# Performance work log

Hardware: AMD Instinct MI355X
Metric: run time of the kernel (lower is better)

The kernel has to match this reference:

```python
import jax, jax.numpy as jnp
import numpy as np

RADIUS = 0.1
NSAMPLE = 64


def ball_query(xyz, new_xyz, pointsnum, radius, nsample):
    """xyz (B,N,2), new_xyz (B,S,2), pointsnum (B,) -> idx (B,S,nsample) int32.
    Mirrors CUDA ball_query: for each query take the first `nsample` point
    indices (in index order) whose squared distance < radius^2 and index <
    pointsnum[b]; slots beyond the number found are padded with the first
    found index (0 if none found)."""
    N = xyz.shape[1]
    # (B,S,N) squared distances
    d2 = jnp.sum((new_xyz[:, :, None, :] - xyz[:, None, :, :]) ** 2, axis=-1)
    valid = jnp.arange(N, dtype=jnp.int32)[None, None, :] < pointsnum[:, None, None]
    mask = (d2 < radius * radius) & valid
    # key = point index if in ball else N (sentinel); smallest `nsample` keys
    key = jnp.where(mask, jnp.arange(N, dtype=jnp.int32), N)
    neg_small, _ = jax.lax.top_k(-key, nsample)          # largest of -key == smallest keys
    sorted_keys = -neg_small                              # ascending in-ball indices, N-padded
    first = sorted_keys[..., :1]
    pad = jnp.where(first < N, first, 0)
    idx = jnp.where(sorted_keys < N, sorted_keys, pad)
    return idx.astype(jnp.int32)


def group(features, idx):
    """features (B,C,N), idx (B,S,K) -> (B,C,S,K)."""
    return jax.vmap(lambda f, i: f[:, i])(features, idx)


def setup_inputs() -> dict:
    key = jax.random.key(0)
    k1, k2, k3 = jax.random.split(key, 3)
    B, N, S, C = 4, 16384, 2048, 64
    xyz = jax.random.uniform(k1, (B, N, 2), dtype=jnp.float32)
    new_xyz = jax.random.uniform(k2, (B, S, 2), dtype=jnp.float32)
    features = jax.random.normal(k3, (B, C, N), dtype=jnp.float32)
    pointsnum = jnp.full((B,), N, dtype=jnp.int32)
    return {"xyz": xyz, "new_xyz": new_xyz, "features": features, "pointsnum": pointsnum}


def reference(xyz, new_xyz, features, pointsnum):
    # QueryAndGroup(radius=RADIUS, nsample=NSAMPLE, use_xyz=True)
    idx = ball_query(xyz, new_xyz, pointsnum, RADIUS, NSAMPLE)  # (B,S,K) int32
    xyz_t = jnp.transpose(xyz, (0, 2, 1))                        # (B,2,N)
    grouped_xyz = group(xyz_t, idx)                              # (B,2,S,K)
    grouped_xyz = grouped_xyz - jnp.transpose(new_xyz, (0, 2, 1))[..., None]
    grouped_features = group(features, idx)                      # (B,C,S,K)
    new_features = jnp.concatenate([grouped_xyz, grouped_features], axis=1)  # (B,2+C,S,K)
    return new_features
```

## Files before the change

### kernel.cpp

```cpp
#include <hip/hip_runtime.h>
#include <stdint.h>

#define B 4
#define N 16384
#define S 2048
#define C 64
#define K 64
#define OC 66
#define R2 0.01f
#define NXCD 8

typedef float f32x4 __attribute__((ext_vector_type(4)));

__global__ __launch_bounds__(256) void transpose_kernel(const float* __restrict__ f,
                                                        float* __restrict__ ft) {
    __shared__ float tile[64 * 65];
    const int n0 = blockIdx.x * 64;
    const int b  = blockIdx.y;
    const int t  = threadIdx.x;

    const int nl = t & 63, cl = t >> 6;
    #pragma unroll
    for (int cc = cl; cc < 64; cc += 4) {
        tile[cc * 65 + nl] = __builtin_nontemporal_load(&f[((size_t)b * C + cc) * N + n0 + nl]);
    }
    __syncthreads();

    const int cl2 = t & 63, nl2 = t >> 6;
    #pragma unroll
    for (int nn = nl2; nn < 64; nn += 4) {
        ft[((size_t)b * N + n0 + nn) * C + cl2] = tile[cl2 * 65 + nn];
    }
}

template <bool USE_T>
__global__ __launch_bounds__(256) void qag_kernel(const float* __restrict__ xyz,
                                                  const float* __restrict__ new_xyz,
                                                  const float* __restrict__ feat,
                                                  const float* __restrict__ ft,
                                                  const int* __restrict__ pointsnum,
                                                  float* __restrict__ out) {
    __shared__ int   s_idx[4][K];
    __shared__ float tile[4][16][K];

    const int t    = threadIdx.x;
    const int lane = t & 63;
    const int wu   = __builtin_amdgcn_readfirstlane(t >> 6);

    const int nwg = (B * S) / 4;
    const int bid = blockIdx.x;
    const int swz = (bid & (NXCD - 1)) * (nwg / NXCD) + (bid >> 3);

    const int q0   = swz * 4;
    const int b    = q0 >> 11;
    const int s0   = q0 & (S - 1);
    const int q    = q0 + wu;
    const int s    = s0 + wu;

    const float qx = new_xyz[(size_t)q * 2 + 0];
    const float qy = new_xyz[(size_t)q * 2 + 1];
    const float* __restrict__ xb = xyz + (size_t)b * N * 2;

    int pn = pointsnum[b];
    pn = pn < 0 ? 0 : (pn > N ? N : pn);
    int cnt = 0;
    for (int base = 0; base < pn && cnt < K; base += 256) {
        float2 p[4];
        #pragma unroll
        for (int u = 0; u < 4; ++u) {
            int i  = base + u * 64 + lane;
            int ic = i < N ? i : N - 1;
            p[u] = *(const float2*)&xb[(size_t)ic * 2];
        }
        #pragma unroll
        for (int u = 0; u < 4; ++u) {
            const int i = base + u * 64 + lane;
            bool ok = false;
            if (i < pn) {
                const float dx = __fsub_rn(qx, p[u].x);
                const float dy = __fsub_rn(qy, p[u].y);
                const float d2 = __fadd_rn(__fmul_rn(dx, dx), __fmul_rn(dy, dy));
                ok = d2 < R2;
            }
            const unsigned long long m = __ballot(ok);
            if (ok) {
                const int pos = cnt + __popcll(m & ((1ull << lane) - 1ull));
                if (pos < K) s_idx[wu][pos] = i;
            }
            cnt += __popcll(m);
        }
    }
    const int found = cnt < K ? cnt : K;
    const int first = (found > 0) ? s_idx[wu][0] : 0;
    const int id    = (lane < found) ? s_idx[wu][lane] : first;

    const size_t SK = (size_t)S * K;
    const float2 pxy = *(const float2*)&xb[(size_t)id * 2];
    {
        float* ob = out + ((size_t)b * OC) * SK + (size_t)s * K;
        __builtin_nontemporal_store(pxy.x - qx, ob + lane);
        __builtin_nontemporal_store(pxy.y - qy, ob + SK + lane);
    }

    const float* __restrict__ row = USE_T ? (ft + ((size_t)b * N + id) * C) : nullptr;
    const float* __restrict__ fb  = feat + (size_t)b * C * N;
    const int ql = lane >> 4;
    const int kq = (lane & 15) * 4;

    #pragma unroll
    for (int cc = 0; cc < 4; ++cc) {
        float4 g0, g1, g2, g3;
        if (USE_T) {
            const float4* r4 = (const float4*)(row + 16 * cc);
            g0 = r4[0]; g1 = r4[1]; g2 = r4[2]; g3 = r4[3];
        } else {
            const int c0 = 16 * cc;
            g0.x = fb[(size_t)(c0 +  0) * N + id]; g0.y = fb[(size_t)(c0 +  1) * N + id];
            g0.z = fb[(size_t)(c0 +  2) * N + id]; g0.w = fb[(size_t)(c0 +  3) * N + id];
            g1.x = fb[(size_t)(c0 +  4) * N + id]; g1.y = fb[(size_t)(c0 +  5) * N + id];
            g1.z = fb[(size_t)(c0 +  6) * N + id]; g1.w = fb[(size_t)(c0 +  7) * N + id];
            g2.x = fb[(size_t)(c0 +  8) * N + id]; g2.y = fb[(size_t)(c0 +  9) * N + id];
            g2.z = fb[(size_t)(c0 + 10) * N + id]; g2.w = fb[(size_t)(c0 + 11) * N + id];
            g3.x = fb[(size_t)(c0 + 12) * N + id]; g3.y = fb[(size_t)(c0 + 13) * N + id];
            g3.z = fb[(size_t)(c0 + 14) * N + id]; g3.w = fb[(size_t)(c0 + 15) * N + id];
        }

        __syncthreads();
        tile[wu][ 0][lane] = g0.x; tile[wu][ 1][lane] = g0.y;
        tile[wu][ 2][lane] = g0.z; tile[wu][ 3][lane] = g0.w;
        tile[wu][ 4][lane] = g1.x; tile[wu][ 5][lane] = g1.y;
        tile[wu][ 6][lane] = g1.z; tile[wu][ 7][lane] = g1.w;
        tile[wu][ 8][lane] = g2.x; tile[wu][ 9][lane] = g2.y;
        tile[wu][10][lane] = g2.z; tile[wu][11][lane] = g2.w;
        tile[wu][12][lane] = g3.x; tile[wu][13][lane] = g3.y;
        tile[wu][14][lane] = g3.z; tile[wu][15][lane] = g3.w;
        __syncthreads();

        #pragma unroll
        for (int j = 0; j < 4; ++j) {
            const int c16 = 4 * wu + j;
            const int c   = 16 * cc + c16;
            f32x4 vv = *(const f32x4*)&tile[ql][c16][kq];
            float* bp = out + ((size_t)b * OC + 2 + c) * SK + (size_t)s0 * K;
            __builtin_nontemporal_store(vv, ((f32x4*)bp) + lane);
        }
    }
}

extern "C" void kernel_launch(void* const* d_in, const int* in_sizes, int n_in,
                              void* d_out, int out_size, void* d_ws, size_t ws_size,
                              hipStream_t stream) {
    const float* xyz       = (const float*)d_in[0];
    const float* new_xyz   = (const float*)d_in[1];
    const float* feat      = (const float*)d_in[2];
    const int*   pointsnum = (const int*)d_in[3];
    float*       out       = (float*)d_out;

    const size_t need = (size_t)B * N * C * sizeof(float);
    if (ws_size >= need) {
        float* ft = (float*)d_ws;
        transpose_kernel<<<dim3(N / 64, B), 256, 0, stream>>>(feat, ft);
        qag_kernel<true><<<B * S / 4, 256, 0, stream>>>(xyz, new_xyz, feat, ft, pointsnum, out);
    } else {
        qag_kernel<false><<<B * S / 4, 256, 0, stream>>>(xyz, new_xyz, feat, nullptr, pointsnum, out);
    }
}
```

Before: 55.91 us.

## Overlap ball query with feature transpose in one prep kernel, gather separately

Merges the feature transpose and the ball-query search into a single prep launch: blocks below 1024 transpose features, and the remaining blocks run the neighbor search and write relative xyz plus the index list to the workspace. A separate gather kernel then reads the indices and scatters the transposed feature rows into the output. The aim is to run the compute-bound search alongside the bandwidth-bound transpose instead of serialising them. The cost is an extra index round-trip through global memory and one more launch boundary before the gather.

```diff
diff --git a/kernel.cpp b/kernel.cpp
--- a/kernel.cpp
+++ b/kernel.cpp
@@ -12,24 +12,139 @@
 
 typedef float f32x4 __attribute__((ext_vector_type(4)));
 
-__global__ __launch_bounds__(256) void transpose_kernel(const float* __restrict__ f,
-                                                        float* __restrict__ ft) {
+__global__ __launch_bounds__(256) void prep_kernel(const float* __restrict__ f,
+                                                   const float* __restrict__ xyz,
+                                                   const float* __restrict__ new_xyz,
+                                                   const int* __restrict__ pointsnum,
+                                                   float* __restrict__ ft,
+                                                   int* __restrict__ idx,
+                                                   float* __restrict__ out) {
     __shared__ float tile[64 * 65];
-    const int n0 = blockIdx.x * 64;
-    const int b  = blockIdx.y;
-    const int t  = threadIdx.x;
-
-    const int nl = t & 63, cl = t >> 6;
+    __shared__ int   s_idx[4][K];
+
+    const int t = threadIdx.x;
+
+    if (blockIdx.x < 1024) {
+        const int n0 = (blockIdx.x & 255) * 64;
+        const int b  = blockIdx.x >> 8;
+
+        const int nl = t & 63, cl = t >> 6;
+        #pragma unroll
+        for (int cc = cl; cc < 64; cc += 4) {
+            tile[cc * 65 + nl] = __builtin_nontemporal_load(&f[((size_t)b * C + cc) * N + n0 + nl]);
+        }
+        __syncthreads();
+
+        const int cl2 = t & 63, nl2 = t >> 6;
+        #pragma unroll
+        for (int nn = nl2; nn < 64; nn += 4) {
+            ft[((size_t)b * N + n0 + nn) * C + cl2] = tile[cl2 * 65 + nn];
+        }
+        return;
+    }
+
+    const int lane = t & 63;
+    const int wu   = __builtin_amdgcn_readfirstlane(t >> 6);
+    const int q0   = (int)(blockIdx.x - 1024) * 4;
+    const int b    = q0 >> 11;
+    const int q    = q0 + wu;
+    const int s    = (q0 & (S - 1)) + wu;
+
+    const float qx = new_xyz[(size_t)q * 2 + 0];
+    const float qy = new_xyz[(size_t)q * 2 + 1];
+    const float* __restrict__ xb = xyz + (size_t)b * N * 2;
+
+    int pn = pointsnum[b];
+    pn = pn < 0 ? 0 : (pn > N ? N : pn);
+    int cnt = 0;
+    for (int base = 0; base < pn && cnt < K; base += 256) {
+        float2 p[4];
+        #pragma unroll
+        for (int u = 0; u < 4; ++u) {
+            int i  = base + u * 64 + lane;
+            int ic = i < N ? i : N - 1;
+            p[u] = *(const float2*)&xb[(size_t)ic * 2];
+        }
+        #pragma unroll
+        for (int u = 0; u < 4; ++u) {
+            const int i = base + u * 64 + lane;
+            bool ok = false;
+            if (i < pn) {
+                const float dx = __fsub_rn(qx, p[u].x);
+                const float dy = __fsub_rn(qy, p[u].y);
+                const float d2 = __fadd_rn(__fmul_rn(dx, dx), __fmul_rn(dy, dy));
+                ok = d2 < R2;
+            }
+            const unsigned long long m = __ballot(ok);
+            if (ok) {
+                const int pos = cnt + __popcll(m & ((1ull << lane) - 1ull));
+                if (pos < K) s_idx[wu][pos] = i;
+            }
+            cnt += __popcll(m);
+        }
+    }
+    const int found = cnt < K ? cnt : K;
+    const int first = (found > 0) ? s_idx[wu][0] : 0;
+    const int id    = (lane < found) ? s_idx[wu][lane] : first;
+
+    idx[(size_t)q * K + lane] = id;
+
+    const size_t SK = (size_t)S * K;
+    const float2 pxy = *(const float2*)&xb[(size_t)id * 2];
+    float* ob = out + ((size_t)b * OC) * SK + (size_t)s * K;
+    __builtin_nontemporal_store(pxy.x - qx, ob + lane);
+    __builtin_nontemporal_store(pxy.y - qy, ob + SK + lane);
+}
+
+__global__ __launch_bounds__(256) void gather_kernel(const float* __restrict__ ft,
+                                                     const int* __restrict__ idx,
+                                                     float* __restrict__ out) {
+    __shared__ float tile[4][16][K];
+
+    const int t    = threadIdx.x;
+    const int lane = t & 63;
+    const int wu   = __builtin_amdgcn_readfirstlane(t >> 6);
+
+    const int nwg = (B * S) / 4;
+    const int bid = blockIdx.x;
+    const int swz = (bid & (NXCD - 1)) * (nwg / NXCD) + (bid >> 3);
+
+    const int q0 = swz * 4;
+    const int b  = q0 >> 11;
+    const int s0 = q0 & (S - 1);
+    const int q  = q0 + wu;
+
+    const int id = idx[(size_t)q * K + lane];
+    const float* __restrict__ row = ft + ((size_t)b * N + id) * C;
+
+    const size_t SK = (size_t)S * K;
+    const int ql = lane >> 4;
+    const int kq = (lane & 15) * 4;
+
     #pragma unroll
-    for (int cc = cl; cc < 64; cc += 4) {
-        tile[cc * 65 + nl] = __builtin_nontemporal_load(&f[((size_t)b * C + cc) * N + n0 + nl]);
-    }
-    __syncthreads();
-
-    const int cl2 = t & 63, nl2 = t >> 6;
-    #pragma unroll
-    for (int nn = nl2; nn < 64; nn += 4) {
-        ft[((size_t)b * N + n0 + nn) * C + cl2] = tile[cl2 * 65 + nn];
+    for (int cc = 0; cc < 4; ++cc) {
+        const float4* r4 = (const float4*)(row + 16 * cc);
+        const float4 g0 = r4[0], g1 = r4[1], g2 = r4[2], g3 = r4[3];
+
+        __syncthreads();
+        tile[wu][ 0][lane] = g0.x; tile[wu][ 1][lane] = g0.y;
+        tile[wu][ 2][lane] = g0.z; tile[wu][ 3][lane] = g0.w;
+        tile[wu][ 4][lane] = g1.x; tile[wu][ 5][lane] = g1.y;
+        tile[wu][ 6][lane] = g1.z; tile[wu][ 7][lane] = g1.w;
+        tile[wu][ 8][lane] = g2.x; tile[wu][ 9][lane] = g2.y;
+        tile[wu][10][lane] = g2.z; tile[wu][11][lane] = g2.w;
+        tile[wu][12][lane] = g3.x; tile[wu][13][lane] = g3.y;
+        tile[wu][14][lane] = g3.z; tile[wu][15][lane] = g3.w;
+        __syncthreads();
+
+        #pragma unroll
+        for (int j = 0; j < 4; ++j) {
+            const int c16 = 4 * wu + j;
+            const int c   = 16 * cc + c16;
+            f32x4 vv = *(const f32x4*)&tile[ql][c16][kq];
+            float* bp = out + ((size_t)b * OC + 2 + c) * SK + (size_t)s0 * K;
+            __builtin_nontemporal_store(vv, ((f32x4*)bp) + lane);
+        }
     }
 }
 
@@ -156,10 +271,17 @@
     const int*   pointsnum = (const int*)d_in[3];
     float*       out       = (float*)d_out;
 
-    const size_t need = (size_t)B * N * C * sizeof(float);
-    if (ws_size >= need) {
+    const size_t ft_bytes  = (size_t)B * N * C * sizeof(float);
+    const size_t idx_bytes = (size_t)B * S * K * sizeof(int);
+
+    if (ws_size >= ft_bytes + idx_bytes) {
+        float* ft  = (float*)d_ws;
+        int*   idx = (int*)((char*)d_ws + ft_bytes);
+        prep_kernel<<<1024 + B * S / 4, 256, 0, stream>>>(feat, xyz, new_xyz, pointsnum, ft, idx, out);
+        gather_kernel<<<B * S / 4, 256, 0, stream>>>(ft, idx, out);
+    } else if (ws_size >= ft_bytes) {
         float* ft = (float*)d_ws;
-        transpose_kernel<<<dim3(N / 64, B), 256, 0, stream>>>(feat, ft);
+        prep_kernel<<<1024, 256, 0, stream>>>(feat, xyz, new_xyz, pointsnum, ft, nullptr, out);
         qag_kernel<true><<<B * S / 4, 256, 0, stream>>>(xyz, new_xyz, feat, ft, pointsnum, out);
     } else {
         qag_kernel<false><<<B * S / 4, 256, 0, stream>>>(xyz, new_xyz, feat, nullptr, pointsnum, out);
```

Result: slower. 59.77 us (+6.9%).
